# Optimization experiments

Measured on AMD Instinct MI355X. Metric: run time of the kernel, lower is better.

## Reference

```python
import jax, jax.numpy as jnp
import numpy as np

B, C, H, W = 32, 128, 12, 12
L = H * W
D = C + 1            # +1 coordinate channel
HID = 64

def leaky(x):
    return jax.nn.leaky_relu(x, negative_slope=0.01)

def setup_inputs() -> dict:
    key = jax.random.key(0)
    ks = jax.random.split(key, 9)
    def lin(k, fin, fout):
        bound = 1.0 / np.sqrt(fin)
        kw, kb = jax.random.split(k)
        Wt = jax.random.uniform(kw, (fin, fout), minval=-bound, maxval=bound, dtype=jnp.float32)
        bb = jax.random.uniform(kb, (fout,), minval=-bound, maxval=bound, dtype=jnp.float32)
        return Wt, bb
    x_img = jax.random.normal(ks[0], (B, C, H, W), dtype=jnp.float32)
    W1, b1 = lin(ks[1], 2 * D, HID)
    W2, b2 = lin(ks[2], HID, HID)
    Wp, bp = lin(ks[3], HID, HID)
    Wo, bo = lin(ks[4], HID, HID)
    return {"x_img": x_img, "W1": W1, "b1": b1, "W2": W2, "b2": b2,
            "Wp": Wp, "bp": bp, "Wo": Wo, "bo": bo}

def reference(x_img, W1, b1, W2, b2, Wp, bp, Wo, bo):
    b, c, h, w = x_img.shape
    length = h * w
    # [b, L, c]
    x = x_img.reshape(b, c, length).transpose(0, 2, 1)
    coords = jnp.broadcast_to(jnp.arange(length, dtype=x.dtype)[None, :, None], (b, length, 1))
    x = jnp.concatenate([x, coords], axis=2)            # [b, L, D]
    # pair feature is concat([x_i, x_j]) where x_i[b,i,j]=x[b,j], x_j[b,i,j]=x[b,i].
    # Linear on concat == split-weight sum; avoids materializing [b,L,L,2D].
    Wa, Wb = W1[:D], W1[D:]
    gi = jnp.einsum('bld,dh->blh', x, Wa)               # contribution of x_i (indexed by j)
    gj = jnp.einsum('bld,dh->blh', x, Wb)               # contribution of x_j (indexed by i)
    g = leaky(gi[:, None, :, :] + gj[:, :, None, :] + b1)   # [b, L, L, HID]
    g = leaky(jnp.einsum('bijh,hk->bijk', g, W2) + b2)       # [b, L, L, HID]
    out = g.sum(axis=(1, 2))                                 # [b, HID]
    out = leaky(out @ Wp + bp)
    out = leaky(out @ Wo + bo)
    return out
```

## Files before the change

kernel.cpp:

```cpp
#include <hip/hip_runtime.h>


#define B_   32
#define C_   128
#define L_   144
#define HID_ 64
#define D_   129
#define STR  68
#define YB_  18
#define PL_  12

typedef __bf16 bf16x8 __attribute__((ext_vector_type(8)));
typedef float  floatx4 __attribute__((ext_vector_type(4)));

__device__ __forceinline__ float leaky(float x) { return fmaxf(x, 0.01f * x); }
__device__ __forceinline__ floatx4 leaky4(floatx4 x) {
    return __builtin_elementwise_max(x, x * 0.01f);
}

__global__ __launch_bounds__(256) void k_proj(const float* __restrict__ x_img,
                                              const float* __restrict__ W1,
                                              const float* __restrict__ b1,
                                              float* __restrict__ gi,
                                              float* __restrict__ gjb)
{
    __shared__ float sW[D_ * HID_];
    const int t     = threadIdx.x;
    const int b     = blockIdx.x >> 1;
    const int which = blockIdx.x & 1;
    const int l0    = blockIdx.y * PL_;

    {
        const floatx4* w4 = (const floatx4*)(W1 + which * (D_ * HID_));
        floatx4* s4 = (floatx4*)sW;
        for (int idx = t; idx < D_ * HID_ / 4; idx += 256)
            s4[idx] = w4[idx];
    }
    __syncthreads();

    const int h    = t & 63;
    const int wave = t >> 6;
    float* outp  = which ? gjb : gi;
    const float bias = which ? b1[h] : 0.f;

#pragma unroll
    for (int il = 0; il < PL_ / 4; ++il) {
        const int l = l0 + wave * (PL_ / 4) + il;
        const float* xp = x_img + (size_t)(b * C_) * L_ + l;

        float a0 = fmaf((float)l, sW[C_ * HID_ + h], bias);
        float a1 = 0.f;
#pragma unroll 4
        for (int c = 0; c < C_; c += 2) {
            a0 = fmaf(xp[c * L_],       sW[c * HID_ + h],       a0);
            a1 = fmaf(xp[(c + 1) * L_], sW[(c + 1) * HID_ + h], a1);
        }
        outp[(b * L_ + l) * HID_ + h] = a0 + a1;
    }
}

__global__ __launch_bounds__(256, 4) void k_pairs(const float* __restrict__ gi,
                                                  const float* __restrict__ gjb,
                                                  const float* __restrict__ W2,
                                                  const float* __restrict__ b2,
                                                  float* __restrict__ partial)
{
    __shared__ float s_gi[L_ * STR];

    const int t    = threadIdx.x;
    const int wave = t >> 6;
    const int lane = t & 63;
    const int m    = lane & 15;
    const int quad = lane >> 4;
    const int b    = blockIdx.x;

    {
        const floatx4* g4i = (const floatx4*)(gi + (size_t)b * (L_ * HID_));
        for (int idx = t; idx < L_ * HID_ / 4; idx += 256) {
            int l  = idx >> 4;
            int c4 = idx & 15;
            *(floatx4*)&s_gi[l * STR + c4 * 4] = g4i[idx];
        }
    }

    bf16x8 Bf[2][4];
#pragma unroll
    for (int kc = 0; kc < 2; ++kc)
#pragma unroll
        for (int nt = 0; nt < 4; ++nt)
#pragma unroll
            for (int j = 0; j < 8; ++j)
                Bf[kc][nt][j] = (__bf16)W2[(kc * 32 + quad * 8 + j) * HID_ + nt * 16 + m];

    float b2v[4];
#pragma unroll
    for (int nt = 0; nt < 4; ++nt) b2v[nt] = b2[nt * 16 + m];

    floatx4 sacc[4];
#pragma unroll
    for (int nt = 0; nt < 4; ++nt) sacc[nt] = floatx4{0.f, 0.f, 0.f, 0.f};

    const int h0 = quad * 8;

    __syncthreads();

#pragma unroll
    for (int ii = 0; ii < 2; ++ii) {
        const int i = (blockIdx.y * 4 + wave) * 2 + ii;

        const float* gjr = gjb + ((size_t)b * L_ + i) * HID_;
        floatx4 gjA0 = *(const floatx4*)(gjr + h0);
        floatx4 gjA1 = *(const floatx4*)(gjr + h0 + 4);
        floatx4 gjB0 = *(const floatx4*)(gjr + 32 + h0);
        floatx4 gjB1 = *(const floatx4*)(gjr + 32 + h0 + 4);

        for (int jt = 0; jt < 9; ++jt) {
            const float* gr = &s_gi[(jt * 16 + m) * STR];

            floatx4 va0 = *(const floatx4*)(gr + h0)          + gjA0;
            floatx4 va1 = *(const floatx4*)(gr + h0 + 4)      + gjA1;
            floatx4 vb0 = *(const floatx4*)(gr + 32 + h0)     + gjB0;
            floatx4 vb1 = *(const floatx4*)(gr + 32 + h0 + 4) + gjB1;
            va0 = leaky4(va0); va1 = leaky4(va1);
            vb0 = leaky4(vb0); vb1 = leaky4(vb1);

            bf16x8 A0, A1;
#pragma unroll
            for (int j = 0; j < 4; ++j) {
                A0[j]     = (__bf16)va0[j];
                A0[4 + j] = (__bf16)va1[j];
                A1[j]     = (__bf16)vb0[j];
                A1[4 + j] = (__bf16)vb1[j];
            }

            floatx4 Cf[4];
#pragma unroll
            for (int nt = 0; nt < 4; ++nt) {
                Cf[nt] = floatx4{0.f, 0.f, 0.f, 0.f};
                Cf[nt] = __builtin_amdgcn_mfma_f32_16x16x32_bf16(A0, Bf[0][nt], Cf[nt], 0, 0, 0);
                Cf[nt] = __builtin_amdgcn_mfma_f32_16x16x32_bf16(A1, Bf[1][nt], Cf[nt], 0, 0, 0);
            }

#pragma unroll
            for (int nt = 0; nt < 4; ++nt)
                sacc[nt] += leaky4(Cf[nt] + b2v[nt]);
        }
    }

    float red[4];
#pragma unroll
    for (int nt = 0; nt < 4; ++nt) {
        float s = sacc[nt][0] + sacc[nt][1] + sacc[nt][2] + sacc[nt][3];
        s += __shfl_xor(s, 16, 64);
        s += __shfl_xor(s, 32, 64);
        red[nt] = s;
    }
    __syncthreads();
    if (quad == 0) {
#pragma unroll
        for (int nt = 0; nt < 4; ++nt)
            s_gi[wave * STR + nt * 16 + m] = red[nt];
    }
    __syncthreads();
    if (t < HID_) {
        float s = s_gi[0 * STR + t] + s_gi[1 * STR + t]
                + s_gi[2 * STR + t] + s_gi[3 * STR + t];
        partial[(b * YB_ + blockIdx.y) * HID_ + t] = s;
    }
}

__global__ __launch_bounds__(64) void k_mlp(const float* __restrict__ partial,
                                            const float* __restrict__ Wp,
                                            const float* __restrict__ bp,
                                            const float* __restrict__ Wo,
                                            const float* __restrict__ bo,
                                            float* __restrict__ out)
{
    __shared__ float s0[HID_], s1[HID_];
    int b = blockIdx.x, k = threadIdx.x;

    float a = 0.f;
#pragma unroll
    for (int yb = 0; yb < YB_; ++yb)
        a += partial[(b * YB_ + yb) * HID_ + k];
    s0[k] = a;
    __syncthreads();

    float v = bp[k];
#pragma unroll 8
    for (int h = 0; h < HID_; ++h) v = fmaf(s0[h], Wp[h * HID_ + k], v);
    v = leaky(v);
    s1[k] = v;
    __syncthreads();
    float w = bo[k];
#pragma unroll 8
    for (int h = 0; h < HID_; ++h) w = fmaf(s1[h], Wo[h * HID_ + k], w);
    w = leaky(w);
    out[b * HID_ + k] = w;
}

extern "C" void kernel_launch(void* const* d_in, const int* in_sizes, int n_in,
                              void* d_out, int out_size, void* d_ws, size_t ws_size,
                              hipStream_t stream)
{
    const float* x_img = (const float*)d_in[0];
    const float* W1    = (const float*)d_in[1];
    const float* b1    = (const float*)d_in[2];
    const float* W2    = (const float*)d_in[3];
    const float* b2    = (const float*)d_in[4];
    const float* Wp    = (const float*)d_in[5];
    const float* bp    = (const float*)d_in[6];
    const float* Wo    = (const float*)d_in[7];
    const float* bo    = (const float*)d_in[8];
    float* out = (float*)d_out;

    float* gi      = (float*)d_ws;
    float* gjb     = gi + B_ * L_ * HID_;
    float* partial = gjb + B_ * L_ * HID_;

    k_proj <<<dim3(B_ * 2, L_ / PL_), 256, 0, stream>>>(x_img, W1, b1, gi, gjb);
    k_pairs<<<dim3(B_, YB_),          256, 0, stream>>>(gi, gjb, W2, b2, partial);
    k_mlp  <<<dim3(B_),                64, 0, stream>>>(partial, Wp, bp, Wo, bo, out);
}
```

Baseline: 106.3 us.

## Fuse final MLP into pairs kernel via last-block atomic counter

Removes the separate k_mlp launch. Each k_pairs block increments a global counter after writing its partial sums, and the last block to finish reduces all partials and runs both small dense layers for every batch. The counter is reset inside k_proj. This saves one kernel launch and its gap, but the final MLP now runs serially on a single 256-thread block instead of 32 blocks, and it adds threadfence and atomic overhead.

```diff
diff --git a/kernel.cpp b/kernel.cpp
--- a/kernel.cpp
+++ b/kernel.cpp
@@ -9,6 +9,7 @@
 #define STR  68
 #define YB_  18
 #define PL_  12
+#define NBLK (B_ * YB_)
 
 typedef __bf16 bf16x8 __attribute__((ext_vector_type(8)));
 typedef float  floatx4 __attribute__((ext_vector_type(4)));
@@ -22,13 +23,17 @@
                                               const float* __restrict__ W1,
                                               const float* __restrict__ b1,
                                               float* __restrict__ gi,
-                                              float* __restrict__ gjb)
+                                              float* __restrict__ gjb,
+                                              int* __restrict__ counter)
 {
     __shared__ float sW[D_ * HID_];
     const int t     = threadIdx.x;
     const int b     = blockIdx.x >> 1;
     const int which = blockIdx.x & 1;
     const int l0    = blockIdx.y * PL_;
+
+    if (blockIdx.x == 0 && blockIdx.y == 0 && t == 0)
+        *counter = 0;
 
     {
         const floatx4* w4 = (const floatx4*)(W1 + which * (D_ * HID_));
@@ -63,9 +68,16 @@
                                                   const float* __restrict__ gjb,
                                                   const float* __restrict__ W2,
                                                   const float* __restrict__ b2,
-                                                  float* __restrict__ partial)
+                                                  const float* __restrict__ Wp,
+                                                  const float* __restrict__ bp,
+                                                  const float* __restrict__ Wo,
+                                                  const float* __restrict__ bo,
+                                                  float* __restrict__ partial,
+                                                  int* __restrict__ counter,
+                                                  float* __restrict__ out)
 {
     __shared__ float s_gi[L_ * STR];
+    __shared__ int   isLast;
 
     const int t    = threadIdx.x;
     const int wave = t >> 6;
@@ -167,36 +179,46 @@
                 + s_gi[2 * STR + t] + s_gi[3 * STR + t];
         partial[(b * YB_ + blockIdx.y) * HID_ + t] = s;
     }
-}
-
-__global__ __launch_bounds__(64) void k_mlp(const float* __restrict__ partial,
-                                            const float* __restrict__ Wp,
-                                            const float* __restrict__ bp,
-                                            const float* __restrict__ Wo,
-                                            const float* __restrict__ bo,
-                                            float* __restrict__ out)
-{
-    __shared__ float s0[HID_], s1[HID_];
-    int b = blockIdx.x, k = threadIdx.x;
-
-    float a = 0.f;
-#pragma unroll
-    for (int yb = 0; yb < YB_; ++yb)
-        a += partial[(b * YB_ + yb) * HID_ + k];
-    s0[k] = a;
-    __syncthreads();
-
-    float v = bp[k];
+
+    __threadfence();
+    __syncthreads();
+    if (t == 0) {
+        int old = atomicAdd(counter, 1);
+        isLast = (old == NBLK - 1);
+    }
+    __syncthreads();
+    if (!isLast) return;
+    __threadfence();
+
+    float* s0 = s_gi;
+    float* s1 = s_gi + B_ * HID_;
+
+    for (int s = t; s < B_ * HID_; s += 256) {
+        int bb = s >> 6, k = s & 63;
+        float a = 0.f;
+#pragma unroll
+        for (int yb = 0; yb < YB_; ++yb)
+            a += partial[(bb * YB_ + yb) * HID_ + k];
+        s0[s] = a;
+    }
+    __syncthreads();
+    for (int s = t; s < B_ * HID_; s += 256) {
+        int bb = s >> 6, k = s & 63;
+        float v = bp[k];
 #pragma unroll 8
-    for (int h = 0; h < HID_; ++h) v = fmaf(s0[h], Wp[h * HID_ + k], v);
-    v = leaky(v);
-    s1[k] = v;
-    __syncthreads();
-    float w = bo[k];
+        for (int h = 0; h < HID_; ++h)
+            v = fmaf(s0[bb * HID_ + h], Wp[h * HID_ + k], v);
+        s1[s] = leaky(v);
+    }
+    __syncthreads();
+    for (int s = t; s < B_ * HID_; s += 256) {
+        int bb = s >> 6, k = s & 63;
+        float w = bo[k];
 #pragma unroll 8
-    for (int h = 0; h < HID_; ++h) w = fmaf(s1[h], Wo[h * HID_ + k], w);
-    w = leaky(w);
-    out[b * HID_ + k] = w;
+        for (int h = 0; h < HID_; ++h)
+            w = fmaf(s1[bb * HID_ + h], Wo[h * HID_ + k], w);
+        out[s] = leaky(w);
+    }
 }
 
 extern "C" void kernel_launch(void* const* d_in, const int* in_sizes, int n_in,
@@ -217,8 +239,9 @@
     float* gi      = (float*)d_ws;
     float* gjb     = gi + B_ * L_ * HID_;
     float* partial = gjb + B_ * L_ * HID_;
-
-    k_proj <<<dim3(B_ * 2, L_ / PL_), 256, 0, stream>>>(x_img, W1, b1, gi, gjb);
-    k_pairs<<<dim3(B_, YB_),          256, 0, stream>>>(gi, gjb, W2, b2, partial);
-    k_mlp  <<<dim3(B_),                64, 0, stream>>>(partial, Wp, bp, Wo, bo, out);
-}
+    int*   counter = (int*)(partial + NBLK * HID_);
+
+    k_proj <<<dim3(B_ * 2, L_ / PL_), 256, 0, stream>>>(x_img, W1, b1, gi, gjb, counter);
+    k_pairs<<<dim3(B_, YB_),          256, 0, stream>>>(gi, gjb, W2, b2, Wp, bp, Wo, bo,
+                                                        partial, counter, out);
+}
```

New measurement: 147.8 us. +39.0%, slower.
